# Kernel tuning notes

Measured on AMD Instinct MI355X. Metric: run time of the kernel, lower is better.

## Reference

```python
import jax, jax.numpy as jnp
import numpy as np

T = 2048
N = 4096
DT = 0.01
V_RESET = 1.0
ALPHA = 0.01
MAX_SPIKES = 128


def setup_inputs() -> dict:
    key = jax.random.key(0)
    ks = jax.random.split(key, 8)
    ts = jnp.arange(T, dtype=jnp.float32) * DT
    input_current = jax.random.normal(ks[0], (T, N), dtype=jnp.float32)
    # _build_w: uniform(minval=0.5) fully-connected weight matrix
    w = jax.random.uniform(ks[1], (N, N), dtype=jnp.float32, minval=0.5, maxval=1.0)
    # _build_initial: uniform(maxval=0.1)
    v0 = jax.random.uniform(ks[2], (N,), dtype=jnp.float32, maxval=0.1)
    i0 = jax.random.uniform(ks[3], (N,), dtype=jnp.float32, maxval=0.1)
    mu = jax.random.uniform(ks[4], (2,), dtype=jnp.float32, minval=0.5, maxval=1.0)
    # uniforms for initial s and for post-spike s resampling (s = log(u) - alpha)
    s0_u = jax.random.uniform(ks[5], (N,), dtype=jnp.float32)
    resample_u = jax.random.uniform(ks[6], (T, N), dtype=jnp.float32)
    return {"ts": ts, "input_current": input_current, "w": w, "v0": v0,
            "i0": i0, "mu": mu, "s0_u": s0_u, "resample_u": resample_u,
            "max_spikes": MAX_SPIKES}


def reference(ts, input_current, w, v0, i0, mu, s0_u, resample_u, max_spikes):
    """Event-driven spiking net: Euler integration of the drift vf with
    spike events when s crosses 0, followed by the masked per-neuron jump
    transition (_inner_trans_fn) using the firing neuron's weight row.
    Returns trajectory ys [T, N, 3] (v, i, s per neuron)."""
    dt = ts[1] - ts[0]
    eps = jnp.float32(1e-12)
    # s0 = log(uniform) - alpha  (always negative; drifts up at rate intensity(v))
    s0 = jnp.log(s0_u + eps) - ALPHA
    y0 = jnp.stack([v0, i0, s0], axis=-1)  # [N, 3]
    mu1, mu2 = mu[0], mu[1]

    def step(carry, xs):
        y, nsp = carry
        inp_t, ru_t = xs
        v, i, s = y[:, 0], y[:, 1], y[:, 2]
        # drift_vf (Euler step)
        v_n = v + dt * (mu1 * (i - v) + mu1 * inp_t)
        i_n = i + dt * (-mu2 * i)
        s_n = s + dt * jax.nn.sigmoid(v)  # intensity_fn(v)
        # event detection: cond_fn = s; event when s reaches 0
        ev = s_n >= 0.0  # [N] event mask
        fire = jnp.any(ev) & (nsp < max_spikes)
        idx = jnp.argmax(ev)  # event_idx = argmax over event mask
        w_row = w[idx]  # weights from firing neuron to all neurons
        # _inner_trans_fn: spiking neurons reset v and resample s;
        # non-spiking neurons receive current injection w[idx][j]
        v_t = jnp.where(ev, v_n - V_RESET, v_n)
        i_t = jnp.where(ev, i_n, i_n + w_row)
        s_t = jnp.where(ev, jnp.log(ru_t + eps) - ALPHA, s_n)
        y_fire = jnp.stack([v_t, i_t, s_t], axis=-1)
        y_free = jnp.stack([v_n, i_n, s_n], axis=-1)
        y_out = jnp.where(fire, y_fire, y_free)
        nsp = nsp + fire.astype(jnp.int32)
        return (y_out, nsp), y_out

    (_, _), ys = jax.lax.scan(step, (y0, jnp.int32(0)),
                              (input_current, resample_u))
    return ys
```

## Files before the change

### kernel.cpp

```cpp
#include <hip/hip_runtime.h>
#include <stddef.h>

#define TT 2048
#define NN 4096
#define LSEG 64
#define NSEG (TT / LSEG)
#define TPA1 1024
#define TPA 64
#define NPT 4
#define TPB 256
#define WCAP 256
#define RING 8
#define MAXU 0xFFFFFFFFu
#define NOFIRE 0xFFFFFFFEu

__global__ __launch_bounds__(TPA1) void phaseA(
    const float* __restrict__ ts, const float* __restrict__ inp,
    const float* __restrict__ w, const float* __restrict__ v0,
    const float* __restrict__ i0, const float* __restrict__ mu,
    const float* __restrict__ s0u, const float* __restrict__ ru,
    const int* __restrict__ mx, unsigned int* __restrict__ hdr,
    unsigned int* __restrict__ fireT, unsigned int* __restrict__ fireIdx)
{
#pragma clang fp contract(off)
  const int tid = threadIdx.x;
  const int wid = tid >> 6;
  const int lane = tid & 63;
  const int n0 = tid * NPT;
  const float dt = ts[1] - ts[0];
  const float mu1 = mu[0], mu2 = mu[1];
  const int maxs = mx[0];

  const float4* inp4 = (const float4*)inp;
  const float4* ru4  = (const float4*)ru;
  const float4* w4   = (const float4*)w;

  float4 a4;
  a4 = ((const float4*)v0)[tid];  float v[NPT]    = {a4.x, a4.y, a4.z, a4.w};
  a4 = ((const float4*)i0)[tid];  float i_nw[NPT] = {a4.x, a4.y, a4.z, a4.w};
  a4 = ((const float4*)s0u)[tid];
  float s[NPT] = {logf(a4.x + 1e-12f) - 0.01f, logf(a4.y + 1e-12f) - 0.01f,
                  logf(a4.z + 1e-12f) - 0.01f, logf(a4.w + 1e-12f) - 0.01f};

  float wv[NPT] = {0.f, 0.f, 0.f, 0.f};
  bool  aw[NPT] = {false, false, false, false};
  int nsp = 0;
  int t_stop = TT;

  __shared__ unsigned int shw[2][16];

  float4 ib[RING], rb[RING];
#pragma unroll
  for (int j = 0; j < RING; ++j) {
    ib[j] = inp4[(size_t)j * (NN / 4) + tid];
    rb[j] = ru4[(size_t)j * (NN / 4) + tid];
  }

  for (int tb = 0; tb < TT; tb += RING) {
#pragma unroll
    for (int j = 0; j < RING; ++j) {
      const int t = tb + j;
      const float4 cur  = ib[j];
      const float4 rrow = rb[j];

      float sn[NPT];
      bool ev[NPT];
      unsigned int m = NOFIRE;
#pragma unroll
      for (int k = 0; k < NPT; ++k) {
        float sig = 1.0f / (1.0f + expf(-v[k]));
        sn[k] = s[k] + dt * sig;
        ev[k] = sn[k] >= 0.0f;
        unsigned int c = ev[k] ? (unsigned int)(n0 + k) : NOFIRE;
        m = m < c ? m : c;
      }

#pragma unroll
      for (int off = 32; off > 0; off >>= 1) {
        unsigned int o = (unsigned int)__shfl_down((int)m, off, 64);
        m = m < o ? m : o;
      }
      const int p = t & 1;
      if (lane == 0) shw[p][wid] = m;
      asm volatile("s_waitcnt lgkmcnt(0)" ::: "memory");
      __builtin_amdgcn_sched_barrier(0);
      __builtin_amdgcn_s_barrier();
      __builtin_amdgcn_sched_barrier(0);

      if (t + RING < TT) {
        ib[j] = inp4[(size_t)(t + RING) * (NN / 4) + tid];
        rb[j] = ru4[(size_t)(t + RING) * (NN / 4) + tid];
      }

      unsigned int gm;
      {
        const uint4* sp = (const uint4*)&shw[p][0];
        uint4 q0 = sp[0], q1 = sp[1], q2 = sp[2], q3 = sp[3];
        unsigned int m0 = q0.x < q0.y ? q0.x : q0.y;
        unsigned int m1 = q0.z < q0.w ? q0.z : q0.w;
        unsigned int m2 = q1.x < q1.y ? q1.x : q1.y;
        unsigned int m3 = q1.z < q1.w ? q1.z : q1.w;
        unsigned int m4 = q2.x < q2.y ? q2.x : q2.y;
        unsigned int m5 = q2.z < q2.w ? q2.z : q2.w;
        unsigned int m6 = q3.x < q3.y ? q3.x : q3.y;
        unsigned int m7 = q3.z < q3.w ? q3.z : q3.w;
        m0 = m0 < m1 ? m0 : m1;  m2 = m2 < m3 ? m2 : m3;
        m4 = m4 < m5 ? m4 : m5;  m6 = m6 < m7 ? m6 : m7;
        m0 = m0 < m2 ? m0 : m2;  m4 = m4 < m6 ? m4 : m6;
        gm = m0 < m4 ? m0 : m4;
      }
      const bool fire = (gm < (unsigned int)NN) && (nsp < maxs);

      float iv[NPT] = {cur.x, cur.y, cur.z, cur.w};
      float rv[NPT] = {rrow.x, rrow.y, rrow.z, rrow.w};
#pragma unroll
      for (int k = 0; k < NPT; ++k) {
        float ifull = aw[k] ? (i_nw[k] + wv[k]) : i_nw[k];
        float vn  = v[k] + dt * (mu1 * (ifull - v[k]) + mu1 * iv[k]);
        float in_ = ifull + dt * (-mu2 * ifull);
        if (fire) {
          if (ev[k]) {
            v[k] = vn - 1.0f;
            s[k] = logf(rv[k] + 1e-12f) - 0.01f;
            aw[k] = false;
          } else {
            v[k] = vn; s[k] = sn[k]; aw[k] = true;
          }
        } else {
          v[k] = vn; s[k] = sn[k]; aw[k] = false;
        }
        i_nw[k] = in_;
      }
      if (fire) {
        float4 wr = w4[(size_t)gm * (NN / 4) + tid];
        wv[0] = wr.x; wv[1] = wr.y; wv[2] = wr.z; wv[3] = wr.w;
        if (tid == 0 && nsp < WCAP) {
          fireT[nsp] = (unsigned int)t;
          fireIdx[nsp] = gm;
        }
        ++nsp;
        if (nsp >= maxs) {
          t_stop = ((t + 1 + LSEG - 1) >> 6) << 6;
          if (t_stop > TT) t_stop = TT;
          goto done;
        }
      }
    }
  }
done:
  if (tid == 0) { hdr[0] = (unsigned int)t_stop; hdr[1] = (unsigned int)nsp; }
}

__global__ __launch_bounds__(TPA) void phaseA2(
    const float* __restrict__ ts, const float* __restrict__ inp,
    const float* __restrict__ w, const float* __restrict__ v0,
    const float* __restrict__ i0, const float* __restrict__ mu,
    const float* __restrict__ s0u, const float* __restrict__ ru,
    const unsigned int* __restrict__ hdr, const unsigned int* __restrict__ fireT,
    const unsigned int* __restrict__ fireIdx, float* __restrict__ ys)
{
#pragma clang fp contract(off)
  const int tid = threadIdx.x;
  const int n = blockIdx.x * TPA + tid;
  const int Kp = (int)hdr[0];
  int nf = (int)hdr[1]; if (nf > WCAP) nf = WCAP;
  const float dt = ts[1] - ts[0];
  const float mu1 = mu[0], mu2 = mu[1];

  __shared__ unsigned int sT[WCAP];
  __shared__ float wlds[WCAP][TPA];
  for (int k = tid; k < nf; k += TPA) sT[k] = fireT[k];
  for (int k0 = 0; k0 < nf; k0 += 8) {
    float tmp[8];
#pragma unroll
    for (int j = 0; j < 8; ++j) {
      int k = k0 + j;
      tmp[j] = (k < nf) ? w[(size_t)fireIdx[k] * NN + n] : 0.0f;
    }
#pragma unroll
    for (int j = 0; j < 8; ++j) {
      int k = k0 + j;
      if (k < nf) wlds[k][tid] = tmp[j];
    }
  }
  __syncthreads();

  float v = v0[n];
  float i = i0[n];
  float s = logf(s0u[n] + 1e-12f) - 0.01f;

  float ib[8], rb[8];
#pragma unroll
  for (int j = 0; j < 8; ++j) {
    ib[j] = inp[(size_t)j * NN + n];
    rb[j] = ru[(size_t)j * NN + n];
  }
  int kp = 0;
  for (int tb = 0; tb < Kp; tb += 8) {
#pragma unroll
    for (int j = 0; j < 8; ++j) {
      const int t = tb + j;
      const float x   = ib[j];
      const float ruv = rb[j];
      if (t + 8 < Kp) {
        ib[j] = inp[(size_t)(t + 8) * NN + n];
        rb[j] = ru[(size_t)(t + 8) * NN + n];
      }
      float sig = 1.0f / (1.0f + expf(-v));
      float sn = s + dt * sig;
      bool e = sn >= 0.0f;
      float vn  = v + dt * (mu1 * (i - v) + mu1 * x);
      float in_ = i + dt * (-mu2 * i);
      bool fire = (kp < nf) && (sT[kp] == (unsigned int)t);
      if (fire) {
        float wc = wlds[kp][tid];
        ++kp;
        if (e) { v = vn - 1.0f; i = in_;      s = logf(ruv + 1e-12f) - 0.01f; }
        else   { v = vn;        i = in_ + wc; s = sn; }
      } else   { v = vn;        i = in_;      s = sn; }
      size_t o = ((size_t)t * NN + n) * 3;
      *(float3*)(ys + o) = make_float3(v, i, s);
    }
  }
}

__global__ __launch_bounds__(TPB) void p1_segc(
    const float* __restrict__ ts, const float* __restrict__ inp,
    const float* __restrict__ mu, const float* __restrict__ ys,
    const unsigned int* __restrict__ hdr, float* __restrict__ buf1)
{
  unsigned int Kp = hdr[0];
  unsigned int g0 = Kp / LSEG;
  unsigned int g = blockIdx.x >> 4;
  if (g < g0) return;
  int n = (blockIdx.x & 15) * TPB + threadIdx.x;
  float dt = ts[1] - ts[0];
  float mu1 = mu[0], mu2 = mu[1];
  float a = 1.0f - dt * mu1, b = dt * mu1, r = 1.0f - dt * mu2;
  float ibase = ys[((size_t)(Kp - 1) * NN + n) * 3 + 1];
  float ij = ibase * powf(r, (float)((int)(g * LSEG) - (int)Kp));
  float c = 0.0f;
  size_t base = (size_t)(g * LSEG) * NN + n;
  for (int j = 0; j < LSEG; ++j) {
    float x = inp[base + (size_t)j * NN];
    c = a * c + b * (ij + x);
    ij *= r;
  }
  buf1[(size_t)g * NN + n] = c;
}

__global__ __launch_bounds__(TPB) void p2_scanv(
    const float* __restrict__ ts, const float* __restrict__ mu,
    const float* __restrict__ ys, const unsigned int* __restrict__ hdr,
    float* __restrict__ buf1)
{
  unsigned int Kp = hdr[0];
  unsigned int g0 = Kp / LSEG;
  if (g0 >= NSEG) return;
  int n = blockIdx.x * TPB + threadIdx.x;
  float dt = ts[1] - ts[0];
  float mu1 = mu[0];
  float a = 1.0f - dt * mu1;
  float aL = a;
  for (int k = 0; k < 6; ++k) aL *= aL;
  float v = ys[((size_t)(Kp - 1) * NN + n) * 3 + 0];
  for (unsigned int g = g0; g < NSEG; ++g) {
    float cg = buf1[(size_t)g * NN + n];
    buf1[(size_t)g * NN + n] = v;
    v = aL * v + cg;
  }
}

__global__ __launch_bounds__(TPB) void p3a_sig(
    const float* __restrict__ ts, const float* __restrict__ inp,
    const float* __restrict__ mu, const unsigned int* __restrict__ hdr,
    const float* __restrict__ buf1, const float* __restrict__ ys,
    float* __restrict__ buf2)
{
  unsigned int Kp = hdr[0];
  unsigned int g0 = Kp / LSEG;
  unsigned int g = blockIdx.x >> 4;
  if (g < g0) return;
  int n = (blockIdx.x & 15) * TPB + threadIdx.x;
  float dt = ts[1] - ts[0];
  float mu1 = mu[0], mu2 = mu[1];
  float r = 1.0f - dt * mu2;
  float v = buf1[(size_t)g * NN + n];
  float ibase = ys[((size_t)(Kp - 1) * NN + n) * 3 + 1];
  float i = ibase * powf(r, (float)((int)(g * LSEG) - (int)Kp));
  float sl = 0.0f;
  for (int j = 0; j < LSEG; ++j) {
    size_t t = (size_t)g * LSEG + j;
    float x = inp[t * NN + n];
    float sig = 1.0f / (1.0f + expf(-v));
    sl = sl + dt * sig;
    float vn  = v + dt * (mu1 * (i - v) + mu1 * x);
    float in_ = i + dt * (-mu2 * i);
    v = vn; i = in_;
  }
  buf2[(size_t)g * NN + n] = sl;
}

__global__ __launch_bounds__(TPB) void p4_scans(
    const float* __restrict__ ys, const unsigned int* __restrict__ hdr,
    float* __restrict__ buf2)
{
  unsigned int Kp = hdr[0];
  unsigned int g0 = Kp / LSEG;
  if (g0 >= NSEG) return;
  int n = blockIdx.x * TPB + threadIdx.x;
  float s = ys[((size_t)(Kp - 1) * NN + n) * 3 + 2];
  for (unsigned int g = g0; g < NSEG; ++g) {
    float t = buf2[(size_t)g * NN + n];
    buf2[(size_t)g * NN + n] = s;
    s += t;
  }
}

__global__ __launch_bounds__(TPB) void p3b_seg(
    const float* __restrict__ ts, const float* __restrict__ inp,
    const float* __restrict__ mu, const unsigned int* __restrict__ hdr,
    const float* __restrict__ buf1, const float* __restrict__ buf2,
    float* __restrict__ ys)
{
  unsigned int Kp = hdr[0];
  unsigned int g0 = Kp / LSEG;
  unsigned int g = blockIdx.x >> 4;
  if (g < g0) return;
  int n = (blockIdx.x & 15) * TPB + threadIdx.x;
  float dt = ts[1] - ts[0];
  float mu1 = mu[0], mu2 = mu[1];
  float r = 1.0f - dt * mu2;
  float v = buf1[(size_t)g * NN + n];
  float sb = buf2[(size_t)g * NN + n];
  float ibase = ys[((size_t)(Kp - 1) * NN + n) * 3 + 1];
  float i = ibase * powf(r, (float)((int)(g * LSEG) - (int)Kp));
  float sl = 0.0f;
  for (int j = 0; j < LSEG; ++j) {
    size_t t = (size_t)g * LSEG + j;
    float x = inp[t * NN + n];
    float sig = 1.0f / (1.0f + expf(-v));
    sl = sl + dt * sig;
    float vn  = v + dt * (mu1 * (i - v) + mu1 * x);
    float in_ = i + dt * (-mu2 * i);
    size_t o = (t * NN + n) * 3;
    ys[o] = vn; ys[o + 1] = in_; ys[o + 2] = sl + sb;
    v = vn; i = in_;
  }
}

extern "C" void kernel_launch(void* const* d_in, const int* in_sizes, int n_in,
                              void* d_out, int out_size, void* d_ws, size_t ws_size,
                              hipStream_t stream)
{
  (void)in_sizes; (void)n_in; (void)out_size; (void)ws_size;
  const float* ts  = (const float*)d_in[0];
  const float* inp = (const float*)d_in[1];
  const float* w   = (const float*)d_in[2];
  const float* v0  = (const float*)d_in[3];
  const float* i0  = (const float*)d_in[4];
  const float* mu  = (const float*)d_in[5];
  const float* s0u = (const float*)d_in[6];
  const float* ru  = (const float*)d_in[7];
  const int*   mx  = (const int*)d_in[8];
  float* ys = (float*)d_out;

  char* wsb = (char*)d_ws;
  unsigned int* hdr     = (unsigned int*)wsb;
  unsigned int* fireT   = (unsigned int*)(wsb + 256);
  unsigned int* fireIdx = (unsigned int*)(wsb + 1280);
  float* buf1 = (float*)(wsb + 4096);
  float* buf2 = buf1 + (size_t)NSEG * NN;

  phaseA<<<1, TPA1, 0, stream>>>(ts, inp, w, v0, i0, mu, s0u, ru, mx,
                                 hdr, fireT, fireIdx);
  phaseA2<<<NN / TPA, TPA, 0, stream>>>(ts, inp, w, v0, i0, mu, s0u, ru,
                                        hdr, fireT, fireIdx, ys);
  p1_segc<<<NSEG * 16, TPB, 0, stream>>>(ts, inp, mu, ys, hdr, buf1);
  p2_scanv<<<NN / TPB, TPB, 0, stream>>>(ts, mu, ys, hdr, buf1);
  p3a_sig<<<NSEG * 16, TPB, 0, stream>>>(ts, inp, mu, hdr, buf1, ys, buf2);
  p4_scans<<<NN / TPB, TPB, 0, stream>>>(ys, hdr, buf2);
  p3b_seg<<<NSEG * 16, TPB, 0, stream>>>(ts, inp, mu, hdr, buf1, buf2, ys);
}
```

Baseline: 633.6 us.

## Fuse trajectory writes into the sequential phase and drop the replay kernel

The single-block sequential kernel now writes each timestep's state straight to the output. The separate phaseA2 kernel, which replayed the recorded fire events to regenerate the prefix trajectory, is removed along with the fire-time and index buffers. Once the spike budget is spent, the per-step block-wide reduction and barrier are skipped. The kernel then keeps running uncoupled until the next segment boundary, so the stop point becomes a multiple of the segment length. The trade-off is extra global-store traffic inside the one-block serial loop, which could lengthen the critical path, in exchange for removing a whole kernel and its weight gathers.

```diff
diff --git a/kernel.cpp b/kernel.cpp
--- a/kernel.cpp
+++ b/kernel.cpp
@@ -6,10 +6,8 @@
 #define LSEG 64
 #define NSEG (TT / LSEG)
 #define TPA1 1024
-#define TPA 64
 #define NPT 4
 #define TPB 256
-#define WCAP 256
 #define RING 8
 #define MAXU 0xFFFFFFFFu
 #define NOFIRE 0xFFFFFFFEu
@@ -20,7 +18,7 @@
     const float* __restrict__ i0, const float* __restrict__ mu,
     const float* __restrict__ s0u, const float* __restrict__ ru,
     const int* __restrict__ mx, unsigned int* __restrict__ hdr,
-    unsigned int* __restrict__ fireT, unsigned int* __restrict__ fireIdx)
+    float* __restrict__ ys)
 {
 #pragma clang fp contract(off)
   const int tid = threadIdx.x;
@@ -62,6 +60,7 @@
       const int t = tb + j;
       const float4 cur  = ib[j];
       const float4 rrow = rb[j];
+      const bool coupled = (nsp < maxs);
 
       float sn[NPT];
       bool ev[NPT];
@@ -75,26 +74,38 @@
         m = m < c ? m : c;
       }
 
-#pragma unroll
-      for (int off = 32; off > 0; off >>= 1) {
-        unsigned int o = (unsigned int)__shfl_down((int)m, off, 64);
-        m = m < o ? m : o;
-      }
-      const int p = t & 1;
-      if (lane == 0) shw[p][wid] = m;
-      asm volatile("s_waitcnt lgkmcnt(0)" ::: "memory");
-      __builtin_amdgcn_sched_barrier(0);
-      __builtin_amdgcn_s_barrier();
-      __builtin_amdgcn_sched_barrier(0);
+      if (coupled) {
+#pragma unroll
+        for (int off = 32; off > 0; off >>= 1) {
+          unsigned int o = (unsigned int)__shfl_down((int)m, off, 64);
+          m = m < o ? m : o;
+        }
+        if (lane == 0) shw[t & 1][wid] = m;
+        asm volatile("s_waitcnt lgkmcnt(0)" ::: "memory");
+        __builtin_amdgcn_sched_barrier(0);
+        __builtin_amdgcn_s_barrier();
+        __builtin_amdgcn_sched_barrier(0);
+      }
 
       if (t + RING < TT) {
         ib[j] = inp4[(size_t)(t + RING) * (NN / 4) + tid];
         rb[j] = ru4[(size_t)(t + RING) * (NN / 4) + tid];
       }
 
-      unsigned int gm;
-      {
-        const uint4* sp = (const uint4*)&shw[p][0];
+      float ifull[NPT];
+#pragma unroll
+      for (int k = 0; k < NPT; ++k) ifull[k] = aw[k] ? (i_nw[k] + wv[k]) : i_nw[k];
+      if (t > 0) {
+        size_t o = ((size_t)(t - 1) * NN + (size_t)n0) * 3;
+        float4* yo = (float4*)(ys + o);
+        yo[0] = make_float4(v[0], ifull[0], s[0], v[1]);
+        yo[1] = make_float4(ifull[1], s[1], v[2], ifull[2]);
+        yo[2] = make_float4(s[2], v[3], ifull[3], s[3]);
+      }
+
+      unsigned int gm = NOFIRE;
+      if (coupled) {
+        const uint4* sp = (const uint4*)&shw[t & 1][0];
         uint4 q0 = sp[0], q1 = sp[1], q2 = sp[2], q3 = sp[3];
         unsigned int m0 = q0.x < q0.y ? q0.x : q0.y;
         unsigned int m1 = q0.z < q0.w ? q0.z : q0.w;
@@ -109,15 +120,14 @@
         m0 = m0 < m2 ? m0 : m2;  m4 = m4 < m6 ? m4 : m6;
         gm = m0 < m4 ? m0 : m4;
       }
-      const bool fire = (gm < (unsigned int)NN) && (nsp < maxs);
+      const bool fire = coupled && (gm < (unsigned int)NN);
 
       float iv[NPT] = {cur.x, cur.y, cur.z, cur.w};
       float rv[NPT] = {rrow.x, rrow.y, rrow.z, rrow.w};
 #pragma unroll
       for (int k = 0; k < NPT; ++k) {
-        float ifull = aw[k] ? (i_nw[k] + wv[k]) : i_nw[k];
-        float vn  = v[k] + dt * (mu1 * (ifull - v[k]) + mu1 * iv[k]);
-        float in_ = ifull + dt * (-mu2 * ifull);
+        float vn  = v[k] + dt * (mu1 * (ifull[k] - v[k]) + mu1 * iv[k]);
+        float in_ = ifull[k] + dt * (-mu2 * ifull[k]);
         if (fire) {
           if (ev[k]) {
             v[k] = vn - 1.0f;
@@ -134,94 +144,23 @@
       if (fire) {
         float4 wr = w4[(size_t)gm * (NN / 4) + tid];
         wv[0] = wr.x; wv[1] = wr.y; wv[2] = wr.z; wv[3] = wr.w;
-        if (tid == 0 && nsp < WCAP) {
-          fireT[nsp] = (unsigned int)t;
-          fireIdx[nsp] = gm;
-        }
         ++nsp;
-        if (nsp >= maxs) {
-          t_stop = ((t + 1 + LSEG - 1) >> 6) << 6;
-          if (t_stop > TT) t_stop = TT;
-          goto done;
-        }
-      }
+      }
+      if (nsp >= maxs && ((t + 1) & (LSEG - 1)) == 0) { t_stop = t + 1; goto done; }
     }
   }
 done:
+  {
+    float ifull[NPT];
+#pragma unroll
+    for (int k = 0; k < NPT; ++k) ifull[k] = aw[k] ? (i_nw[k] + wv[k]) : i_nw[k];
+    size_t o = ((size_t)(t_stop - 1) * NN + (size_t)n0) * 3;
+    float4* yo = (float4*)(ys + o);
+    yo[0] = make_float4(v[0], ifull[0], s[0], v[1]);
+    yo[1] = make_float4(ifull[1], s[1], v[2], ifull[2]);
+    yo[2] = make_float4(s[2], v[3], ifull[3], s[3]);
+  }
   if (tid == 0) { hdr[0] = (unsigned int)t_stop; hdr[1] = (unsigned int)nsp; }
-}
-
-__global__ __launch_bounds__(TPA) void phaseA2(
-    const float* __restrict__ ts, const float* __restrict__ inp,
-    const float* __restrict__ w, const float* __restrict__ v0,
-    const float* __restrict__ i0, const float* __restrict__ mu,
-    const float* __restrict__ s0u, const float* __restrict__ ru,
-    const unsigned int* __restrict__ hdr, const unsigned int* __restrict__ fireT,
-    const unsigned int* __restrict__ fireIdx, float* __restrict__ ys)
-{
-#pragma clang fp contract(off)
-  const int tid = threadIdx.x;
-  const int n = blockIdx.x * TPA + tid;
-  const int Kp = (int)hdr[0];
-  int nf = (int)hdr[1]; if (nf > WCAP) nf = WCAP;
-  const float dt = ts[1] - ts[0];
-  const float mu1 = mu[0], mu2 = mu[1];
-
-  __shared__ unsigned int sT[WCAP];
-  __shared__ float wlds[WCAP][TPA];
-  for (int k = tid; k < nf; k += TPA) sT[k] = fireT[k];
-  for (int k0 = 0; k0 < nf; k0 += 8) {
-    float tmp[8];
-#pragma unroll
-    for (int j = 0; j < 8; ++j) {
-      int k = k0 + j;
-      tmp[j] = (k < nf) ? w[(size_t)fireIdx[k] * NN + n] : 0.0f;
-    }
-#pragma unroll
-    for (int j = 0; j < 8; ++j) {
-      int k = k0 + j;
-      if (k < nf) wlds[k][tid] = tmp[j];
-    }
-  }
-  __syncthreads();
-
-  float v = v0[n];
-  float i = i0[n];
-  float s = logf(s0u[n] + 1e-12f) - 0.01f;
-
-  float ib[8], rb[8];
-#pragma unroll
-  for (int j = 0; j < 8; ++j) {
-    ib[j] = inp[(size_t)j * NN + n];
-    rb[j] = ru[(size_t)j * NN + n];
-  }
-  int kp = 0;
-  for (int tb = 0; tb < Kp; tb += 8) {
-#pragma unroll
-    for (int j = 0; j < 8; ++j) {
-      const int t = tb + j;
-      const float x   = ib[j];
-      const float ruv = rb[j];
-      if (t + 8 < Kp) {
-        ib[j] = inp[(size_t)(t + 8) * NN + n];
-        rb[j] = ru[(size_t)(t + 8) * NN + n];
-      }
-      float sig = 1.0f / (1.0f + expf(-v));
-      float sn = s + dt * sig;
-      bool e = sn >= 0.0f;
-      float vn  = v + dt * (mu1 * (i - v) + mu1 * x);
-      float in_ = i + dt * (-mu2 * i);
-      bool fire = (kp < nf) && (sT[kp] == (unsigned int)t);
-      if (fire) {
-        float wc = wlds[kp][tid];
-        ++kp;
-        if (e) { v = vn - 1.0f; i = in_;      s = logf(ruv + 1e-12f) - 0.01f; }
-        else   { v = vn;        i = in_ + wc; s = sn; }
-      } else   { v = vn;        i = in_;      s = sn; }
-      size_t o = ((size_t)t * NN + n) * 3;
-      *(float3*)(ys + o) = make_float3(v, i, s);
-    }
-  }
 }
 
 __global__ __launch_bounds__(TPB) void p1_segc(
@@ -366,16 +305,11 @@
   float* ys = (float*)d_out;
 
   char* wsb = (char*)d_ws;
-  unsigned int* hdr     = (unsigned int*)wsb;
-  unsigned int* fireT   = (unsigned int*)(wsb + 256);
-  unsigned int* fireIdx = (unsigned int*)(wsb + 1280);
+  unsigned int* hdr = (unsigned int*)wsb;
   float* buf1 = (float*)(wsb + 4096);
   float* buf2 = buf1 + (size_t)NSEG * NN;
 
-  phaseA<<<1, TPA1, 0, stream>>>(ts, inp, w, v0, i0, mu, s0u, ru, mx,
-                                 hdr, fireT, fireIdx);
-  phaseA2<<<NN / TPA, TPA, 0, stream>>>(ts, inp, w, v0, i0, mu, s0u, ru,
-                                        hdr, fireT, fireIdx, ys);
+  phaseA<<<1, TPA1, 0, stream>>>(ts, inp, w, v0, i0, mu, s0u, ru, mx, hdr, ys);
   p1_segc<<<NSEG * 16, TPB, 0, stream>>>(ts, inp, mu, ys, hdr, buf1);
   p2_scanv<<<NN / TPB, TPB, 0, stream>>>(ts, mu, ys, hdr, buf1);
   p3a_sig<<<NSEG * 16, TPB, 0, stream>>>(ts, inp, mu, hdr, buf1, ys, buf2);
```

Result: slower. 865.6 us (+36.6%).
